# Optimization experiments

Measured on AMD Instinct MI355X. Metric: run time of the kernel, lower is better.

The kernel has to match this reference:

```python
import jax, jax.numpy as jnp
import numpy as np

# ---- static config (matches init_kwargs) ----
D_MODEL = 2048
D_STATE = 64
D_CONV = 4
EXPAND = 2
HEADDIM = 64
NGROUPS = 1
CHUNK = 256
D_INNER = EXPAND * D_MODEL            # 4096
NHEADS = D_INNER // HEADDIM           # 64
CONV_DIM = D_INNER + 2 * NGROUPS * D_STATE   # 4224
D_IN_PROJ = 2 * D_INNER + 2 * NGROUPS * D_STATE + NHEADS  # 8384
EPS = 1e-5


def setup_inputs() -> dict:
    key = jax.random.key(0)
    ks = jax.random.split(key, 7)
    B, L = 2, 2048
    u = jax.random.normal(ks[0], (B, L, D_MODEL), jnp.float32)
    W_in = jax.random.normal(ks[1], (D_IN_PROJ, D_MODEL), jnp.float32) * (D_MODEL ** -0.5)
    conv_w = jax.random.normal(ks[2], (CONV_DIM, D_CONV), jnp.float32) * (D_CONV ** -0.5)
    conv_b = jnp.zeros((CONV_DIM,), jnp.float32)
    # dt_bias = softplus^{-1}(dt) with dt ~ LogUniform(1e-3, 1e-1), as in the torch init
    dt = jnp.exp(jax.random.uniform(ks[3], (NHEADS,), jnp.float32)
                 * (np.log(0.1) - np.log(0.001)) + np.log(0.001))
    dt_bias = dt + jnp.log(-jnp.expm1(-dt))
    A_log = jnp.log(jax.random.uniform(ks[4], (NHEADS,), jnp.float32, minval=1.0, maxval=16.0))
    D = jnp.ones((NHEADS,), jnp.float32)
    norm_w = jnp.ones((D_INNER,), jnp.float32)
    W_out = jax.random.normal(ks[5], (D_MODEL, D_INNER), jnp.float32) * (D_INNER ** -0.5)
    return dict(u=u, W_in=W_in, conv_w=conv_w, conv_b=conv_b, dt_bias=dt_bias,
                A_log=A_log, D=D, norm_w=norm_w, W_out=W_out)


def _chunked_ssd(x, dt, A, Bm, Cm):
    """Mamba2 chunked selective scan (ssd, discrete form).
    x:[b,l,h,p] dt:[b,l,h] A:[h] Bm,Cm:[b,l,n] (ngroups=1, broadcast over heads).
    Returns y:[b,l,h,p]."""
    b, l, h, p = x.shape
    c = l // CHUNK
    xc = x.reshape(b, c, CHUNK, h, p)
    dtc = dt.reshape(b, c, CHUNK, h)
    Bc = Bm.reshape(b, c, CHUNK, D_STATE)
    Cc = Cm.reshape(b, c, CHUNK, D_STATE)

    Abar = (dtc * A).transpose(0, 3, 1, 2)          # [b,h,c,s]
    Acum = jnp.cumsum(Abar, axis=-1)                # [b,h,c,s]

    # intra-chunk decay matrix L[i,j] = exp(sum_{k=j+1..i} Abar_k), lower-tri
    seg = Acum[..., :, None] - Acum[..., None, :]   # [b,h,c,s,s]
    tri = jnp.tril(jnp.ones((CHUNK, CHUNK), bool))
    Lmat = jnp.where(tri, jnp.exp(seg), 0.0)

    xdt = xc * dtc[..., None]                       # [b,c,s,h,p] (dt*B*x discretization)
    Y_diag = jnp.einsum('bcln,bcsn,bhcls,bcshp->bclhp', Cc, Bc, Lmat, xdt)

    # per-chunk final states
    decay_states = jnp.exp(Acum[..., -1:] - Acum)   # [b,h,c,s]
    states = jnp.einsum('bcsn,bhcs,bcshp->bchpn', Bc, decay_states, xdt)

    # inter-chunk recurrence (associative scan across chunk summaries)
    Achunk = Acum[..., -1]                          # [b,h,c]
    Acs = jnp.cumsum(jnp.pad(Achunk, ((0, 0), (0, 0), (1, 0))), axis=-1)  # [b,h,c+1]
    segc = Acs[..., :, None] - Acs[..., None, :]
    tric = jnp.tril(jnp.ones((c + 1, c + 1), bool))
    decay_chunk = jnp.where(tric, jnp.exp(segc), 0.0)          # [b,h,c+1,c+1]
    states0 = jnp.pad(states, ((0, 0), (1, 0), (0, 0), (0, 0), (0, 0)))  # zero init state
    new_states = jnp.einsum('bhzc,bchpn->bzhpn', decay_chunk, states0)
    prev_states = new_states[:, :-1]                # state entering each chunk [b,c,h,p,n]

    state_decay = jnp.exp(Acum)                     # [b,h,c,s]
    Y_off = jnp.einsum('bcln,bchpn,bhcl->bclhp', Cc, prev_states, state_decay)
    return (Y_diag + Y_off).reshape(b, l, h, p)


def reference(u, W_in, conv_w, conv_b, dt_bias, A_log, D, norm_w, W_out):
    b, l, _ = u.shape
    zxbcdt = u @ W_in.T                                        # [b,l,8384]
    z = zxbcdt[..., :D_INNER]
    xBC = zxbcdt[..., D_INNER:D_INNER + CONV_DIM]
    dt = jax.nn.softplus(zxbcdt[..., D_INNER + CONV_DIM:] + dt_bias)  # [b,l,h]

    # causal depthwise conv1d + SiLU
    xp = jnp.pad(xBC, ((0, 0), (D_CONV - 1, 0), (0, 0)))
    xBC = conv_b + sum(xp[:, w:w + l, :] * conv_w[:, w] for w in range(D_CONV))
    xBC = jax.nn.silu(xBC)

    x = xBC[..., :D_INNER].reshape(b, l, NHEADS, HEADDIM)
    Bm = xBC[..., D_INNER:D_INNER + D_STATE]
    Cm = xBC[..., D_INNER + D_STATE:]

    A = -jnp.exp(A_log)                                        # [h]
    y = _chunked_ssd(x, dt, A, Bm, Cm)                         # [b,l,h,p]
    y = y + x * D[None, None, :, None]                         # D skip on raw x
    y = y.reshape(b, l, D_INNER)

    # gated RMSNorm (norm_before_gate=False): gate first, then normalize
    y = y * jax.nn.silu(z)
    y = y * jax.lax.rsqrt(jnp.mean(y * y, axis=-1, keepdims=True) + EPS) * norm_w
    return y @ W_out.T
```

## Files before the change

kernel.cpp:

```cpp
#include <hip/hip_runtime.h>
#include <hip/hip_bf16.h>
#include <cstdint>

#define DPROJ  8384

typedef __attribute__((ext_vector_type(8))) short short8;
typedef __attribute__((ext_vector_type(4))) short sh4;
typedef __attribute__((ext_vector_type(2))) short sh2;
typedef __attribute__((ext_vector_type(4))) float f32x4;

#define ZX16_OFF   0ul
#define DTB_OFF    17170432ul
#define ACU_OFF    17432576ul
#define CBT_OFF    17694720ul
#define ST_OFF     18219008ul
#define YB_OFF     22413312ul
#define HALO_OFF   39190528ul
#define U16_OFF    39393280ul
#define WIN16_OFF  43587584ul
#define WOUT16_OFF 39393280ul

__device__ __forceinline__ short f2bf(float x) {
  union { float f; uint32_t u; } v{x};
  uint32_t r = (v.u + 0x7fff + ((v.u >> 16) & 1)) >> 16;
  return (short)r;
}
__device__ __forceinline__ float bf2f(short s) {
  union { uint32_t u; float f; } v;
  v.u = ((uint32_t)(uint16_t)s) << 16;
  return v.f;
}

__global__ __launch_bounds__(256) void cast_bf16_kernel(
    const float* __restrict__ in, short* __restrict__ out, int n8) {
  int i = blockIdx.x * 256 + threadIdx.x;
  if (i >= n8) return;
  const float4* p = (const float4*)(in + (size_t)i * 8);
  float4 a = p[0], b = p[1];
  short8 o;
  o[0] = f2bf(a.x); o[1] = f2bf(a.y); o[2] = f2bf(a.z); o[3] = f2bf(a.w);
  o[4] = f2bf(b.x); o[5] = f2bf(b.y); o[6] = f2bf(b.z); o[7] = f2bf(b.w);
  *(short8*)(out + (size_t)i * 8) = o;
}

__device__ __forceinline__ void gload16(const void* g, const void* l) {
  __builtin_amdgcn_global_load_lds(
      (const __attribute__((address_space(1))) void*)g,
      (__attribute__((address_space(3))) void*)l, 16, 0, 0);
}

template <int OUTBF>
__global__ __launch_bounds__(512) void gemm_big(
    const short* __restrict__ A, int lda, const short* __restrict__ B, int ldb,
    void* __restrict__ Cv, int ldc, int K, int Nvalid) {
  const int orig = blockIdx.x + gridDim.x * blockIdx.y;
  const int xcd = orig & 7;
  const int cid = orig >> 3;
  const int rpx = gridDim.y >> 3;
  const int tn = cid / rpx;
  const int tm = xcd * rpx + (cid % rpx);
  __shared__ __align__(16) short As[256 * 64];
  __shared__ __align__(16) short Bs[128 * 64];
  const int t = threadIdx.x;
  const int w = t >> 6, lane = t & 63;
  const int m0 = tm * 256, n0 = tn * 128;
  const int wr = (w >> 1) * 64, wc = (w & 1) * 64;
  const int fr = lane & 15;
  const int cik = lane >> 4;
  const int frs = fr & 7;
  const int rl = t >> 3;
  const int sch = ((t & 7) ^ (rl & 7)) << 3;
  const short* pa_[4];
  const short* pb_[2];
#pragma unroll
  for (int c = 0; c < 4; ++c)
    pa_[c] = A + (size_t)(m0 + c * 64 + rl) * lda + sch;
#pragma unroll
  for (int c = 0; c < 2; ++c) {
    int br = n0 + c * 64 + rl;
    if (br > Nvalid - 1) br = Nvalid - 1;
    pb_[c] = B + (size_t)br * ldb + sch;
  }
  f32x4 acc[4][4];
#pragma unroll
  for (int i = 0; i < 4; ++i)
#pragma unroll
    for (int j = 0; j < 4; ++j) acc[i][j] = (f32x4){0.f, 0.f, 0.f, 0.f};

  for (int k0 = 0; k0 < K; k0 += 64) {
#pragma unroll
    for (int c = 0; c < 4; ++c)
      gload16(pa_[c] + k0, &As[c * 4096 + w * 512 + lane * 8]);
#pragma unroll
    for (int c = 0; c < 2; ++c)
      gload16(pb_[c] + k0, &Bs[c * 4096 + w * 512 + lane * 8]);
    __syncthreads();
#pragma unroll
    for (int kk = 0; kk < 2; ++kk) {
      const int ci = kk * 4 + cik;
      short8 af[4], bg[4];
#pragma unroll
      for (int i = 0; i < 4; ++i) {
        const int ra = wr + i * 16 + fr;
        const int rb = wc + i * 16 + fr;
        af[i] = *(const short8*)&As[ra * 64 + ((ci ^ frs) << 3)];
        bg[i] = *(const short8*)&Bs[rb * 64 + ((ci ^ frs) << 3)];
      }
#pragma unroll
      for (int i = 0; i < 4; ++i)
#pragma unroll
        for (int j = 0; j < 4; ++j)
          acc[i][j] = __builtin_amdgcn_mfma_f32_16x16x32_bf16(af[i], bg[j],
                                                              acc[i][j], 0, 0, 0);
    }
    __syncthreads();
  }
#pragma unroll
  for (int i = 0; i < 4; ++i) {
    const int row = m0 + wr + i * 16 + (lane >> 4) * 4;
#pragma unroll
    for (int j = 0; j < 4; ++j) {
      const int col = n0 + wc + j * 16 + fr;
      if (col < Nvalid) {
#pragma unroll
        for (int r = 0; r < 4; ++r) {
          if (OUTBF)
            ((short*)Cv)[(size_t)(row + r) * ldc + col] = f2bf(acc[i][j][r]);
          else
            ((float*)Cv)[(size_t)(row + r) * ldc + col] = acc[i][j][r];
        }
      }
    }
  }
}

template <int OUTBF>
__global__ __launch_bounds__(256) void gemm_bf16(
    const short* __restrict__ A, int lda, const short* __restrict__ B, int ldb,
    void* __restrict__ Cv, int ldc, int K, int Nvalid) {
  const int orig = blockIdx.x + gridDim.x * blockIdx.y;
  const int xcd = orig & 7;
  const int cid = orig >> 3;
  const int rpx = gridDim.y >> 3;
  const int tn = cid / rpx;
  const int tm = xcd * rpx + (cid % rpx);
  __shared__ __align__(16) short As[128 * 64];
  __shared__ __align__(16) short Bs[128 * 64];
  const int t = threadIdx.x;
  const int w = t >> 6, lane = t & 63;
  const int m0 = tm * 128, n0 = tn * 128;
  const int wr = (w >> 1) * 64, wc = (w & 1) * 64;
  const int fr = lane & 15;
  const int cik = lane >> 4;
  const int frs = fr & 7;
  const int rl = lane >> 3;
  const int sch = ((lane & 7) ^ rl) << 3;
  const short* pa_[4];
  const short* pb_[4];
#pragma unroll
  for (int c = 0; c < 4; ++c) {
    int r = c * 32 + w * 8 + rl;
    pa_[c] = A + (size_t)(m0 + r) * lda + sch;
    int br = n0 + r;
    if (br > Nvalid - 1) br = Nvalid - 1;
    pb_[c] = B + (size_t)br * ldb + sch;
  }
  f32x4 acc[4][4];
#pragma unroll
  for (int i = 0; i < 4; ++i)
#pragma unroll
    for (int j = 0; j < 4; ++j) acc[i][j] = (f32x4){0.f, 0.f, 0.f, 0.f};

  for (int k0 = 0; k0 < K; k0 += 64) {
#pragma unroll
    for (int c = 0; c < 4; ++c) {
      gload16(pa_[c] + k0, &As[c * 2048 + w * 512 + lane * 8]);
      gload16(pb_[c] + k0, &Bs[c * 2048 + w * 512 + lane * 8]);
    }
    __syncthreads();
#pragma unroll
    for (int kk = 0; kk < 2; ++kk) {
      const int ci = kk * 4 + cik;
      short8 af[4], bg[4];
#pragma unroll
      for (int i = 0; i < 4; ++i) {
        const int ra = wr + i * 16 + fr;
        const int rb = wc + i * 16 + fr;
        af[i] = *(const short8*)&As[ra * 64 + ((ci ^ frs) << 3)];
        bg[i] = *(const short8*)&Bs[rb * 64 + ((ci ^ frs) << 3)];
      }
#pragma unroll
      for (int i = 0; i < 4; ++i)
#pragma unroll
        for (int j = 0; j < 4; ++j)
          acc[i][j] = __builtin_amdgcn_mfma_f32_16x16x32_bf16(af[i], bg[j],
                                                              acc[i][j], 0, 0, 0);
    }
    __syncthreads();
  }
#pragma unroll
  for (int i = 0; i < 4; ++i) {
    const int row = m0 + wr + i * 16 + (lane >> 4) * 4;
#pragma unroll
    for (int j = 0; j < 4; ++j) {
      const int col = n0 + wc + j * 16 + fr;
      if (col < Nvalid) {
#pragma unroll
        for (int r = 0; r < 4; ++r) {
          if (OUTBF)
            ((short*)Cv)[(size_t)(row + r) * ldc + col] = f2bf(acc[i][j][r]);
          else
            ((float*)Cv)[(size_t)(row + r) * ldc + col] = acc[i][j][r];
        }
      }
    }
  }
}

__global__ __launch_bounds__(256) void halo_kernel(const short* __restrict__ zx,
                                                   short* __restrict__ halo) {
  int idx = blockIdx.x * 256 + threadIdx.x;
  int ch = idx % 4224;
  int r = idx / 4224;
  int j = r % 3;
  int r2 = r / 3;
  int lc = r2 & 15, b = r2 >> 4;
  int l = lc * 128 - 3 + j;
  halo[idx] = (l < 0) ? (short)0 : zx[(size_t)(b * 2048 + l) * DPROJ + 4096 + ch];
}

__global__ __launch_bounds__(256) void conv_kernel(short* __restrict__ zx,
                                                   const short* __restrict__ halo,
                                                   const float* __restrict__ cw,
                                                   const float* __restrict__ cb) {
  int idx = blockIdx.x * 256 + threadIdx.x;
  int chp = idx % 2112;
  int r = idx / 2112;
  int ch = chp * 2;
  int lc = r & 15, b = r >> 4;
  float w0a = cw[ch * 4 + 0], w1a = cw[ch * 4 + 1], w2a = cw[ch * 4 + 2],
        w3a = cw[ch * 4 + 3];
  float w0b = cw[ch * 4 + 4], w1b = cw[ch * 4 + 5], w2b = cw[ch * 4 + 6],
        w3b = cw[ch * 4 + 7];
  float ba = cb[ch], bb = cb[ch + 1];
  const short* hp = halo + (size_t)r * 3 * 4224 + ch;
  sh2 h0 = *(const sh2*)hp;
  sh2 h1 = *(const sh2*)(hp + 4224);
  sh2 h2 = *(const sh2*)(hp + 8448);
  float xa3 = bf2f(h0[0]), xb3 = bf2f(h0[1]);
  float xa2 = bf2f(h1[0]), xb2 = bf2f(h1[1]);
  float xa1 = bf2f(h2[0]), xb1 = bf2f(h2[1]);
  size_t base = (size_t)(b * 2048 + lc * 128) * DPROJ + 4096 + ch;
  for (int i = 0; i < 128; ++i) {
    sh2 xv = *(const sh2*)&zx[base];
    float xa0 = bf2f(xv[0]), xb0 = bf2f(xv[1]);
    float va = ba + w0a * xa3 + w1a * xa2 + w2a * xa1 + w3a * xa0;
    float vb = bb + w0b * xb3 + w1b * xb2 + w2b * xb1 + w3b * xb0;
    va = va / (1.f + __expf(-va));
    vb = vb / (1.f + __expf(-vb));
    sh2 o;
    o[0] = f2bf(va);
    o[1] = f2bf(vb);
    *(sh2*)&zx[base] = o;
    xa3 = xa2; xa2 = xa1; xa1 = xa0;
    xb3 = xb2; xb2 = xb1; xb1 = xb0;
    base += DPROJ;
  }
}

__global__ __launch_bounds__(256) void dtacum_kernel(
    const short* __restrict__ zx, const float* __restrict__ dt_bias,
    const float* __restrict__ A_log, float* __restrict__ dtb,
    float* __restrict__ acu) {
  int bid = blockIdx.x;
  int c = bid & 7, h = (bid >> 3) & 63, b = bid >> 9;
  int s = threadIdx.x;
  int tok = b * 2048 + c * 256 + s;
  float raw = bf2f(zx[(size_t)tok * DPROJ + 8320 + h]) + dt_bias[h];
  float dtv = (raw > 20.f) ? raw : log1pf(expf(raw));
  float A = -expf(A_log[h]);
  __shared__ float sc[256];
  sc[s] = dtv * A;
  __syncthreads();
  for (int off = 1; off < 256; off <<= 1) {
    float v = (s >= off) ? sc[s - off] : 0.f;
    __syncthreads();
    sc[s] += v;
    __syncthreads();
  }
  int o = (b * 64 + h) * 2048 + c * 256 + s;
  dtb[o] = dtv;
  acu[o] = sc[s];
}

__global__ __launch_bounds__(256) void cbt_kernel(const short* __restrict__ zx,
                                                  short* __restrict__ cbtT) {
  __shared__ float cl[256][33];
  __shared__ float blds[16][32];
  int bid = blockIdx.x;
  int sb = bid & 15, c = (bid >> 4) & 7, b = bid >> 7;
  int t = threadIdx.x;
  int tok0 = b * 2048 + c * 256;
  float acc[16];
#pragma unroll
  for (int i = 0; i < 16; ++i) acc[i] = 0.f;
  for (int nh = 0; nh < 2; ++nh) {
    __syncthreads();
    for (int it = 0; it < 32; ++it) {
      int e = it * 256 + t;
      int row = e >> 5, n = e & 31;
      cl[row][n] = bf2f(zx[(size_t)(tok0 + row) * DPROJ + 8256 + nh * 32 + n]);
    }
    for (int it = 0; it < 2; ++it) {
      int e = it * 256 + t;
      int row = e >> 5, n = e & 31;
      blds[row][n] =
          bf2f(zx[(size_t)(tok0 + sb * 16 + row) * DPROJ + 8192 + nh * 32 + n]);
    }
    __syncthreads();
    for (int n = 0; n < 32; ++n) {
      float cv = cl[t][n];
#pragma unroll
      for (int s2 = 0; s2 < 16; ++s2) acc[s2] += cv * blds[s2][n];
    }
  }
  short* outp = cbtT + ((size_t)(b * 8 + c) * 256 + t) * 256 + sb * 16;
#pragma unroll
  for (int s2 = 0; s2 < 16; ++s2) outp[s2] = f2bf(acc[s2]);
}

__global__ __launch_bounds__(256) void states_mfma(
    const short* __restrict__ zx, const float* __restrict__ dtb,
    const float* __restrict__ acu, float* __restrict__ st) {
  __shared__ __align__(16) short As2[64][136];
  __shared__ __align__(16) short Bs2[64][136];
  __shared__ float wl[256];
  int bid = blockIdx.x;
  int h = bid & 63, c = (bid >> 6) & 7, b = bid >> 9;
  int t = threadIdx.x;
  int w = t >> 6, lane = t & 63;
  int tok0 = b * 2048 + c * 256;
  int bh = (b * 64 + h) * 2048 + c * 256;
  {
    float aend = acu[bh + 255];
    wl[t] = __expf(aend - acu[bh + t]) * dtb[bh + t];
  }
  __syncthreads();
  const short* xbase = zx + (size_t)tok0 * DPROJ + 4096 + h * 64;
  const short* bbase = zx + (size_t)tok0 * DPROJ + 8192;
  const int fr = lane & 15, fko = (lane >> 4) * 8;
  const int wi = (w >> 1) * 32, wj = (w & 1) * 32;
  f32x4 acc[2][2];
#pragma unroll
  for (int i = 0; i < 2; ++i)
#pragma unroll
    for (int j = 0; j < 2; ++j) acc[i][j] = (f32x4){0.f, 0.f, 0.f, 0.f};

  for (int ph = 0; ph < 2; ++ph) {
    const int kb = ph * 128;
    if (ph) __syncthreads();
    for (int it = 0; it < 8; ++it) {
      int idx = it * 256 + t;
      int p = idx & 63, kg = idx >> 6;
      int k = kb + kg * 4;
      const short* xp = xbase + (size_t)k * DPROJ + p;
      const short* bp = bbase + (size_t)k * DPROJ + p;
      sh4 oa, ob;
#pragma unroll
      for (int r = 0; r < 4; ++r) {
        oa[r] = xp[(size_t)r * DPROJ];
        ob[r] = f2bf(bf2f(bp[(size_t)r * DPROJ]) * wl[k + r]);
      }
      *(sh4*)&As2[p][kg * 4] = oa;
      *(sh4*)&Bs2[p][kg * 4] = ob;
    }
    __syncthreads();
#pragma unroll
    for (int kk0 = 0; kk0 < 128; kk0 += 32) {
      short8 af[2], bg[2];
#pragma unroll
      for (int i = 0; i < 2; ++i) {
        af[i] = *(const short8*)&As2[wi + i * 16 + fr][kk0 + fko];
        bg[i] = *(const short8*)&Bs2[wj + i * 16 + fr][kk0 + fko];
      }
#pragma unroll
      for (int i = 0; i < 2; ++i)
#pragma unroll
        for (int j = 0; j < 2; ++j)
          acc[i][j] = __builtin_amdgcn_mfma_f32_16x16x32_bf16(af[i], bg[j],
                                                              acc[i][j], 0, 0, 0);
    }
  }
  float* out = st + ((size_t)(b * 8 + c) * 64 + h) * 4096;
  const int rq = (lane >> 4) * 4;
#pragma unroll
  for (int i = 0; i < 2; ++i) {
    int p0 = wi + i * 16 + rq;
#pragma unroll
    for (int j = 0; j < 2; ++j) {
      int n = wj + j * 16 + fr;
#pragma unroll
      for (int r = 0; r < 4; ++r)
        out[(size_t)(p0 + r) * 64 + n] = acc[i][j][r];
    }
  }
}

__global__ __launch_bounds__(256) void chunkscan_kernel(
    const float* __restrict__ acu, float* __restrict__ st) {
  int bid = blockIdx.x;
  int pc = bid & 15, h = (bid >> 4) & 63, b = bid >> 10;
  int pn = pc * 256 + threadIdx.x;
  int abase = (b * 64 + h) * 2048;
  float run = 0.f;
  for (int c = 0; c < 8; ++c) {
    size_t idx = ((size_t)(b * 8 + c) * 64 + h) * 4096 + pn;
    float s = st[idx];
    st[idx] = run;
    float ach = acu[abase + c * 256 + 255];
    run = run * __expf(ach) + s;
  }
}

__global__ __launch_bounds__(256) void ydiag_mfma(
    const short* __restrict__ zx, const float* __restrict__ dtb,
    const float* __restrict__ acu, const short* __restrict__ cbtT,
    const float* __restrict__ st, const float* __restrict__ Dp,
    short* __restrict__ yb) {
  __shared__ __align__(16) short Xs[64][328];
  __shared__ float acs[256];
  __shared__ float dts[256];
  int bid = blockIdx.x;
  int h = bid & 63, c = (bid >> 6) & 7, b = bid >> 9;
  int t = threadIdx.x;
  int w = t >> 6, lane = t & 63;
  int tok0 = b * 2048 + c * 256;
  int bh = (b * 64 + h) * 2048 + c * 256;
  acs[t] = acu[bh + t];
  dts[t] = dtb[bh + t];
  const short* xbase = zx + (size_t)tok0 * DPROJ + 4096 + h * 64;
  const float* st_b = st + ((size_t)(b * 8 + c) * 64 + h) * 4096;
  for (int it = 0; it < 16; ++it) {
    int idx = it * 256 + t;
    int p = idx & 63, kg = idx >> 6;
    const short* xp = xbase + (size_t)(kg * 4) * DPROJ + p;
    sh4 o;
    o[0] = xp[0];
    o[1] = xp[DPROJ];
    o[2] = xp[2 * DPROJ];
    o[3] = xp[3 * DPROJ];
    *(sh4*)&Xs[p][kg * 4] = o;
  }
  for (int it = 0; it < 4; ++it) {
    int idx = it * 256 + t;
    int ng = idx & 15, p = idx >> 4;
    float4 v = *(const float4*)&st_b[p * 64 + ng * 4];
    sh4 o;
    o[0] = f2bf(v.x); o[1] = f2bf(v.y); o[2] = f2bf(v.z); o[3] = f2bf(v.w);
    *(sh4*)&Xs[p][256 + ng * 4] = o;
  }
  __syncthreads();

  const int fr = lane & 15, fko = (lane >> 4) * 8;
  float Al[4], eAl[4];
#pragma unroll
  for (int i = 0; i < 4; ++i) {
    Al[i] = acs[(i * 4 + w) * 16 + fr];
    eAl[i] = __expf(Al[i]);
  }
  f32x4 acc[4][4];
#pragma unroll
  for (int i = 0; i < 4; ++i)
#pragma unroll
    for (int j = 0; j < 4; ++j) acc[i][j] = (f32x4){0.f, 0.f, 0.f, 0.f};

  const short* cbt_b = cbtT + (size_t)(b * 8 + c) * 65536;

  const int k0max = (12 + w) * 16 + 16;
  for (int k0 = 0; k0 < k0max; k0 += 32) {
    short8 bg[4];
#pragma unroll
    for (int j = 0; j < 4; ++j)
      bg[j] = *(const short8*)&Xs[j * 16 + fr][k0 + fko];
    const int bi = (k0 + 32 < 256) ? (k0 + 32) : 255;
    const float base = acs[bi];
    float vd[8];
#pragma unroll
    for (int jj = 0; jj < 8; ++jj) {
      int s = k0 + fko + jj;
      vd[jj] = __expf(base - acs[s]) * dts[s];
    }
#pragma unroll
    for (int i = 0; i < 4; ++i) {
      const int li0 = (i * 4 + w) * 16;
      if (k0 > li0 + 15) continue;
      const int l = li0 + fr;
      const short8 cb = *(const short8*)&cbt_b[(size_t)l * 256 + k0 + fko];
      short8 af;
      if (k0 + 32 <= li0) {
        const float u = __expf(Al[i] - base);
#pragma unroll
        for (int jj = 0; jj < 8; ++jj)
          af[jj] = f2bf(bf2f(cb[jj]) * (vd[jj] * u));
      } else {
#pragma unroll
        for (int jj = 0; jj < 8; ++jj) {
          int s = k0 + fko + jj;
          float wv = 0.f;
          if (s <= l) wv = bf2f(cb[jj]) * __expf(Al[i] - acs[s]) * dts[s];
          af[jj] = f2bf(wv);
        }
      }
#pragma unroll
      for (int j = 0; j < 4; ++j)
        acc[i][j] = __builtin_amdgcn_mfma_f32_16x16x32_bf16(af, bg[j],
                                                            acc[i][j], 0, 0, 0);
    }
  }
#pragma unroll
  for (int k0 = 256; k0 < 320; k0 += 32) {
    short8 bg[4];
#pragma unroll
    for (int j = 0; j < 4; ++j)
      bg[j] = *(const short8*)&Xs[j * 16 + fr][k0 + fko];
#pragma unroll
    for (int i = 0; i < 4; ++i) {
      const int l = (i * 4 + w) * 16 + fr;
      const short8 cv = *(const short8*)(zx + (size_t)(tok0 + l) * DPROJ +
                                         8256 + (k0 - 256) + fko);
      short8 af;
#pragma unroll
      for (int jj = 0; jj < 8; ++jj) af[jj] = f2bf(bf2f(cv[jj]) * eAl[i]);
#pragma unroll
      for (int j = 0; j < 4; ++j)
        acc[i][j] = __builtin_amdgcn_mfma_f32_16x16x32_bf16(af, bg[j],
                                                            acc[i][j], 0, 0, 0);
    }
  }
  float Dh = Dp[h];
  const int rq = (lane >> 4) * 4;
#pragma unroll
  for (int i = 0; i < 4; ++i) {
    int l0 = (i * 4 + w) * 16 + rq;
#pragma unroll
    for (int j = 0; j < 4; ++j) {
      int p = j * 16 + fr;
      sh4 x4 = *(const sh4*)&Xs[p][l0];
      f32x4 a = acc[i][j];
#pragma unroll
      for (int r = 0; r < 4; ++r)
        yb[(size_t)(bh + l0 + r) * 64 + p] = f2bf(a[r] + Dh * bf2f(x4[r]));
    }
  }
}

__global__ __launch_bounds__(256) void gatenorm_kernel(
    short* zx, const float* __restrict__ nw, const short* __restrict__ yb) {
  int tok = blockIdx.x;
  int b = tok >> 11, l = tok & 2047;
  int t = threadIdx.x;
  float g[16];
  float ss = 0.f;
#pragma unroll
  for (int i = 0; i < 8; ++i) {
    int d = i * 512 + 2 * t;
    int h = d >> 6, p = d & 63;
    sh2 yv2 = *(const sh2*)&yb[((size_t)(b * 64 + h) * 2048 + l) * 64 + p];
    sh2 zv2 = *(const sh2*)&zx[(size_t)tok * DPROJ + d];
#pragma unroll
    for (int e = 0; e < 2; ++e) {
      float yv = bf2f(yv2[e]);
      float zv = bf2f(zv2[e]);
      float gv = yv * (zv / (1.f + __expf(-zv)));
      g[2 * i + e] = gv;
      ss += gv * gv;
    }
  }
  for (int off = 32; off > 0; off >>= 1) ss += __shfl_down(ss, off);
  __shared__ float red[4];
  int wid = t >> 6, lane = t & 63;
  if (lane == 0) red[wid] = ss;
  __syncthreads();
  float tot = red[0] + red[1] + red[2] + red[3];
  float scale = rsqrtf(tot * (1.f / 4096.f) + 1e-5f);
#pragma unroll
  for (int i = 0; i < 8; ++i) {
    int d = i * 512 + 2 * t;
    sh2 o;
    o[0] = f2bf(g[2 * i] * scale * nw[d]);
    o[1] = f2bf(g[2 * i + 1] * scale * nw[d + 1]);
    *(sh2*)&zx[(size_t)tok * DPROJ + d] = o;
  }
}

extern "C" void kernel_launch(void* const* d_in, const int* in_sizes, int n_in,
                              void* d_out, int out_size, void* d_ws,
                              size_t ws_size, hipStream_t stream) {
  const float* u = (const float*)d_in[0];
  const float* W_in = (const float*)d_in[1];
  const float* conv_w = (const float*)d_in[2];
  const float* conv_b = (const float*)d_in[3];
  const float* dt_bias = (const float*)d_in[4];
  const float* A_log = (const float*)d_in[5];
  const float* Dp = (const float*)d_in[6];
  const float* norm_w = (const float*)d_in[7];
  const float* W_out = (const float*)d_in[8];
  float* out = (float*)d_out;
  float* ws = (float*)d_ws;

  short* zx16 = (short*)(ws + ZX16_OFF);
  float* dtb = ws + DTB_OFF;
  float* acu = ws + ACU_OFF;
  short* cbtT = (short*)(ws + CBT_OFF);
  float* st = ws + ST_OFF;
  short* yb = (short*)(ws + YB_OFF);
  short* halo = (short*)(ws + HALO_OFF);
  short* u16 = (short*)(ws + U16_OFF);
  short* win16 = (short*)(ws + WIN16_OFF);
  short* wout16 = (short*)(ws + WOUT16_OFF);

  cast_bf16_kernel<<<4096, 256, 0, stream>>>(u, u16, 1048576);
  cast_bf16_kernel<<<8384, 256, 0, stream>>>(W_in, win16, 2146304);
  gemm_big<1><<<dim3(66, 16), 512, 0, stream>>>(u16, 2048, win16, 2048, zx16,
                                                DPROJ, 2048, DPROJ);
  halo_kernel<<<1584, 256, 0, stream>>>(zx16, halo);
  conv_kernel<<<264, 256, 0, stream>>>(zx16, halo, conv_w, conv_b);
  dtacum_kernel<<<1024, 256, 0, stream>>>(zx16, dt_bias, A_log, dtb, acu);
  cbt_kernel<<<256, 256, 0, stream>>>(zx16, cbtT);
  states_mfma<<<1024, 256, 0, stream>>>(zx16, dtb, acu, st);
  chunkscan_kernel<<<2048, 256, 0, stream>>>(acu, st);
  ydiag_mfma<<<1024, 256, 0, stream>>>(zx16, dtb, acu, cbtT, st, Dp, yb);
  cast_bf16_kernel<<<4096, 256, 0, stream>>>(W_out, wout16, 1048576);
  gatenorm_kernel<<<4096, 256, 0, stream>>>(zx16, norm_w, yb);
  gemm_bf16<0><<<dim3(16, 32), 256, 0, stream>>>(zx16, DPROJ, wout16, 4096, out,
                                                 2048, 4096, 2048);
}
```

Baseline: 436.5 us.

## Use 256x256 tile GEMM for in-projection, larger tiles for out-proj, vectorize gatenorm

Adds a 512-thread 256x256-tile GEMM kernel for the input projection, halving the grid and raising arithmetic intensity per LDS load. The output projection switches from the 128x128 kernel to the existing 256x128 kernel, and the old gemm_bf16 is removed. The gated RMSNorm kernel now loads and stores 16 contiguous bf16 per thread with 128-bit accesses instead of scattered 32-bit pairs. Larger tiles raise register pressure and lower occupancy. Out-proj now has only 256 blocks, which may underfill the GPU.

```diff
diff --git a/kernel.cpp b/kernel.cpp
--- a/kernel.cpp
+++ b/kernel.cpp
@@ -47,6 +47,95 @@
   __builtin_amdgcn_global_load_lds(
       (const __attribute__((address_space(1))) void*)g,
       (__attribute__((address_space(3))) void*)l, 16, 0, 0);
+}
+
+template <int OUTBF>
+__global__ __launch_bounds__(512) void gemm_huge(
+    const short* __restrict__ A, int lda, const short* __restrict__ B, int ldb,
+    void* __restrict__ Cv, int ldc, int K, int Nvalid) {
+  const int orig = blockIdx.x + gridDim.x * blockIdx.y;
+  const int xcd = orig & 7;
+  const int cid = orig >> 3;
+  const int rpx = gridDim.y >> 3;
+  const int tn = cid / rpx;
+  const int tm = xcd * rpx + (cid % rpx);
+  __shared__ __align__(16) short As[256 * 64];
+  __shared__ __align__(16) short Bs[256 * 64];
+  const int t = threadIdx.x;
+  const int w = t >> 6, lane = t & 63;
+  const int wm = w >> 2, wn = w & 3;
+  const int m0 = tm * 256, n0 = tn * 256;
+  const int fr = lane & 15;
+  const int cik = lane >> 4;
+  const int frs = fr & 7;
+  const int rl = t >> 3;
+  const int sch = ((t & 7) ^ (rl & 7)) << 3;
+  const short* pa_[4];
+  const short* pb_[4];
+#pragma unroll
+  for (int c = 0; c < 4; ++c) {
+    pa_[c] = A + (size_t)(m0 + c * 64 + rl) * lda + sch;
+    int br = n0 + c * 64 + rl;
+    if (br > Nvalid - 1) br = Nvalid - 1;
+    pb_[c] = B + (size_t)br * ldb + sch;
+  }
+  f32x4 acc[8][4];
+#pragma unroll
+  for (int i = 0; i < 8; ++i)
+#pragma unroll
+    for (int j = 0; j < 4; ++j) acc[i][j] = (f32x4){0.f, 0.f, 0.f, 0.f};
+
+  for (int k0 = 0; k0 < K; k0 += 64) {
+#pragma unroll
+    for (int c = 0; c < 4; ++c) {
+      gload16(pa_[c] + k0, &As[c * 4096 + w * 512 + lane * 8]);
+      gload16(pb_[c] + k0, &Bs[c * 4096 + w * 512 + lane * 8]);
+    }
+    __syncthreads();
+#pragma unroll
+    for (int kk = 0; kk < 2; ++kk) {
+      const int ci = kk * 4 + cik;
+      short8 bg[4];
+#pragma unroll
+      for (int j = 0; j < 4; ++j) {
+        const int rb = wn * 64 + j * 16 + fr;
+        bg[j] = *(const short8*)&Bs[rb * 64 + ((ci ^ (rb & 7)) << 3)];
+      }
+#pragma unroll
+      for (int io = 0; io < 2; ++io) {
+        short8 af[4];
+#pragma unroll
+        for (int ii = 0; ii < 4; ++ii) {
+          const int ra = wm * 128 + (io * 4 + ii) * 16 + fr;
+          af[ii] = *(const short8*)&As[ra * 64 + ((ci ^ (ra & 7)) << 3)];
+        }
+#pragma unroll
+        for (int ii = 0; ii < 4; ++ii)
+#pragma unroll
+          for (int j = 0; j < 4; ++j)
+            acc[io * 4 + ii][j] = __builtin_amdgcn_mfma_f32_16x16x32_bf16(
+                af[ii], bg[j], acc[io * 4 + ii][j], 0, 0, 0);
+      }
+    }
+    __syncthreads();
+  }
+#pragma unroll
+  for (int i = 0; i < 8; ++i) {
+    const int row = m0 + wm * 128 + i * 16 + (lane >> 4) * 4;
+#pragma unroll
+    for (int j = 0; j < 4; ++j) {
+      const int col = n0 + wn * 64 + j * 16 + fr;
+      if (col < Nvalid) {
+#pragma unroll
+        for (int r = 0; r < 4; ++r) {
+          if (OUTBF)
+            ((short*)Cv)[(size_t)(row + r) * ldc + col] = f2bf(acc[i][j][r]);
+          else
+            ((float*)Cv)[(size_t)(row + r) * ldc + col] = acc[i][j][r];
+        }
+      }
+    }
+  }
 }
 
 template <int OUTBF>
@@ -94,89 +183,6 @@
 #pragma unroll
     for (int c = 0; c < 2; ++c)
       gload16(pb_[c] + k0, &Bs[c * 4096 + w * 512 + lane * 8]);
-    __syncthreads();
-#pragma unroll
-    for (int kk = 0; kk < 2; ++kk) {
-      const int ci = kk * 4 + cik;
-      short8 af[4], bg[4];
-#pragma unroll
-      for (int i = 0; i < 4; ++i) {
-        const int ra = wr + i * 16 + fr;
-        const int rb = wc + i * 16 + fr;
-        af[i] = *(const short8*)&As[ra * 64 + ((ci ^ frs) << 3)];
-        bg[i] = *(const short8*)&Bs[rb * 64 + ((ci ^ frs) << 3)];
-      }
-#pragma unroll
-      for (int i = 0; i < 4; ++i)
-#pragma unroll
-        for (int j = 0; j < 4; ++j)
-          acc[i][j] = __builtin_amdgcn_mfma_f32_16x16x32_bf16(af[i], bg[j],
-                                                              acc[i][j], 0, 0, 0);
-    }
-    __syncthreads();
-  }
-#pragma unroll
-  for (int i = 0; i < 4; ++i) {
-    const int row = m0 + wr + i * 16 + (lane >> 4) * 4;
-#pragma unroll
-    for (int j = 0; j < 4; ++j) {
-      const int col = n0 + wc + j * 16 + fr;
-      if (col < Nvalid) {
-#pragma unroll
-        for (int r = 0; r < 4; ++r) {
-          if (OUTBF)
-            ((short*)Cv)[(size_t)(row + r) * ldc + col] = f2bf(acc[i][j][r]);
-          else
-            ((float*)Cv)[(size_t)(row + r) * ldc + col] = acc[i][j][r];
-        }
-      }
-    }
-  }
-}
-
-template <int OUTBF>
-__global__ __launch_bounds__(256) void gemm_bf16(
-    const short* __restrict__ A, int lda, const short* __restrict__ B, int ldb,
-    void* __restrict__ Cv, int ldc, int K, int Nvalid) {
-  const int orig = blockIdx.x + gridDim.x * blockIdx.y;
-  const int xcd = orig & 7;
-  const int cid = orig >> 3;
-  const int rpx = gridDim.y >> 3;
-  const int tn = cid / rpx;
-  const int tm = xcd * rpx + (cid % rpx);
-  __shared__ __align__(16) short As[128 * 64];
-  __shared__ __align__(16) short Bs[128 * 64];
-  const int t = threadIdx.x;
-  const int w = t >> 6, lane = t & 63;
-  const int m0 = tm * 128, n0 = tn * 128;
-  const int wr = (w >> 1) * 64, wc = (w & 1) * 64;
-  const int fr = lane & 15;
-  const int cik = lane >> 4;
-  const int frs = fr & 7;
-  const int rl = lane >> 3;
-  const int sch = ((lane & 7) ^ rl) << 3;
-  const short* pa_[4];
-  const short* pb_[4];
-#pragma unroll
-  for (int c = 0; c < 4; ++c) {
-    int r = c * 32 + w * 8 + rl;
-    pa_[c] = A + (size_t)(m0 + r) * lda + sch;
-    int br = n0 + r;
-    if (br > Nvalid - 1) br = Nvalid - 1;
-    pb_[c] = B + (size_t)br * ldb + sch;
-  }
-  f32x4 acc[4][4];
-#pragma unroll
-  for (int i = 0; i < 4; ++i)
-#pragma unroll
-    for (int j = 0; j < 4; ++j) acc[i][j] = (f32x4){0.f, 0.f, 0.f, 0.f};
-
-  for (int k0 = 0; k0 < K; k0 += 64) {
-#pragma unroll
-    for (int c = 0; c < 4; ++c) {
-      gload16(pa_[c] + k0, &As[c * 2048 + w * 512 + lane * 8]);
-      gload16(pb_[c] + k0, &Bs[c * 2048 + w * 512 + lane * 8]);
-    }
     __syncthreads();
 #pragma unroll
     for (int kk = 0; kk < 2; ++kk) {
@@ -559,22 +565,22 @@
   int tok = blockIdx.x;
   int b = tok >> 11, l = tok & 2047;
   int t = threadIdx.x;
+  const int d0 = t * 16;
+  const int h = d0 >> 6, p0 = d0 & 63;
+  short8 yv8[2], zv8[2];
+  yv8[0] = *(const short8*)&yb[((size_t)(b * 64 + h) * 2048 + l) * 64 + p0];
+  yv8[1] = *(const short8*)&yb[((size_t)(b * 64 + h) * 2048 + l) * 64 + p0 + 8];
+  zv8[0] = *(const short8*)&zx[(size_t)tok * DPROJ + d0];
+  zv8[1] = *(const short8*)&zx[(size_t)tok * DPROJ + d0 + 8];
   float g[16];
   float ss = 0.f;
 #pragma unroll
-  for (int i = 0; i < 8; ++i) {
-    int d = i * 512 + 2 * t;
-    int h = d >> 6, p = d & 63;
-    sh2 yv2 = *(const sh2*)&yb[((size_t)(b * 64 + h) * 2048 + l) * 64 + p];
-    sh2 zv2 = *(const sh2*)&zx[(size_t)tok * DPROJ + d];
-#pragma unroll
-    for (int e = 0; e < 2; ++e) {
-      float yv = bf2f(yv2[e]);
-      float zv = bf2f(zv2[e]);
-      float gv = yv * (zv / (1.f + __expf(-zv)));
-      g[2 * i + e] = gv;
-      ss += gv * gv;
-    }
+  for (int i = 0; i < 16; ++i) {
+    float yv = bf2f(yv8[i >> 3][i & 7]);
+    float zv = bf2f(zv8[i >> 3][i & 7]);
+    float gv = yv * (zv / (1.f + __expf(-zv)));
+    g[i] = gv;
+    ss += gv * gv;
   }
   for (int off = 32; off > 0; off >>= 1) ss += __shfl_down(ss, off);
   __shared__ float red[4];
@@ -583,14 +589,12 @@
   __syncthreads();
   float tot = red[0] + red[1] + red[2] + red[3];
   float scale = rsqrtf(tot * (1.f / 4096.f) + 1e-5f);
-#pragma unroll
-  for (int i = 0; i < 8; ++i) {
-    int d = i * 512 + 2 * t;
-    sh2 o;
-    o[0] = f2bf(g[2 * i] * scale * nw[d]);
-    o[1] = f2bf(g[2 * i + 1] * scale * nw[d + 1]);
-    *(sh2*)&zx[(size_t)tok * DPROJ + d] = o;
-  }
+  short8 o[2];
+#pragma unroll
+  for (int i = 0; i < 16; ++i)
+    o[i >> 3][i & 7] = f2bf(g[i] * scale * nw[d0 + i]);
+  *(short8*)&zx[(size_t)tok * DPROJ + d0] = o[0];
+  *(short8*)&zx[(size_t)tok * DPROJ + d0 + 8] = o[1];
 }
 
 extern "C" void kernel_launch(void* const* d_in, const int* in_sizes, int n_in,
@@ -621,8 +625,8 @@
 
   cast_bf16_kernel<<<4096, 256, 0, stream>>>(u, u16, 1048576);
   cast_bf16_kernel<<<8384, 256, 0, stream>>>(W_in, win16, 2146304);
-  gemm_big<1><<<dim3(66, 16), 512, 0, stream>>>(u16, 2048, win16, 2048, zx16,
-                                                DPROJ, 2048, DPROJ);
+  gemm_huge<1><<<dim3(33, 16), 512, 0, stream>>>(u16, 2048, win16, 2048, zx16,
+                                                 DPROJ, 2048, DPROJ);
   halo_kernel<<<1584, 256, 0, stream>>>(zx16, halo);
   conv_kernel<<<264, 256, 0, stream>>>(zx16, halo, conv_w, conv_b);
   dtacum_kernel<<<1024, 256, 0, stream>>>(zx16, dt_bias, A_log, dtb, acu);
@@ -632,6 +636,6 @@
   ydiag_mfma<<<1024, 256, 0, stream>>>(zx16, dtb, acu, cbtT, st, Dp, yb);
   cast_bf16_kernel<<<4096, 256, 0, stream>>>(W_out, wout16, 1048576);
   gatenorm_kernel<<<4096, 256, 0, stream>>>(zx16, norm_w, yb);
-  gemm_bf16<0><<<dim3(16, 32), 256, 0, stream>>>(zx16, DPROJ, wout16, 4096, out,
-                                                 2048, 4096, 2048);
-}
+  gemm_big<0><<<dim3(16, 16), 512, 0, stream>>>(zx16, DPROJ, wout16, 4096, out,
+                                                2048, 4096, 2048);
+}
```

Measured after the change: 474.5 us. 1.09x slower.
